# Performance work log

Measured on AMD Instinct MI355X. Metric: run time of the kernel, lower is better.

## Reference

```python
import jax, jax.numpy as jnp
import numpy as np
from jax import lax

B = 64            # batch size
IMG = 128         # image H=W
C_IN = 3          # channels (also conv kernel size in original code)
Q_DIM = 11
A_DIM = 10
CONV = [24, 24, 24, 24]
KS = 3
EPS = 1e-5
G_IN = (CONV[-1] + 2) * 2 + Q_DIM  # 63


def _lin_init(key, fin, fout):
    kw, kb = jax.random.split(key)
    w = jax.random.normal(kw, (fin, fout), jnp.float32) / np.sqrt(fin).astype(np.float32)
    b = jax.random.normal(kb, (fout,), jnp.float32) * 0.01
    return w, b


def _conv_init(key, cin, cout):
    kw, kb = jax.random.split(key)
    w = jax.random.normal(kw, (cout, cin, KS, KS), jnp.float32) / np.sqrt(cin * KS * KS).astype(np.float32)
    b = jax.random.normal(kb, (cout,), jnp.float32) * 0.01
    return w, b


def setup_inputs() -> dict:
    key = jax.random.key(0)
    ks = jax.random.split(key, 16)
    inp = {
        'img': jax.random.normal(ks[0], (B, C_IN, IMG, IMG), jnp.float32),
        'q': jax.random.normal(ks[1], (B, Q_DIM), jnp.float32),
    }
    cins = [C_IN] + CONV[:-1]
    for li in range(4):
        w, b = _conv_init(ks[2 + li], cins[li], CONV[li])
        inp[f'cw{li+1}'], inp[f'cb{li+1}'] = w, b
        inp[f'bg{li+1}'] = jnp.ones((CONV[li],), jnp.float32)
        inp[f'bb{li+1}'] = jnp.zeros((CONV[li],), jnp.float32)
    gins = [G_IN, 256, 256, 256]
    for li in range(4):
        w, b = _lin_init(ks[6 + li], gins[li], 256)
        inp[f'gw{li+1}'], inp[f'gb{li+1}'] = w, b
    fins, fouts = [256, 256, 256], [256, 256, A_DIM]
    for li in range(3):
        w, b = _lin_init(ks[10 + li], fins[li], fouts[li])
        inp[f'fw{li+1}'], inp[f'fb{li+1}'] = w, b
    return inp


def _conv_block(x, w, b, g, bb):
    # conv(stride=2, pad=1) -> relu -> batchnorm (train-mode batch stats)
    x = lax.conv_general_dilated(x, w, (2, 2), [(1, 1), (1, 1)],
                                 dimension_numbers=('NCHW', 'OIHW', 'NCHW'))
    x = jax.nn.relu(x + b[None, :, None, None])
    m = jnp.mean(x, axis=(0, 2, 3), keepdims=True)
    v = jnp.var(x, axis=(0, 2, 3), keepdims=True)
    return g[None, :, None, None] * (x - m) * jax.lax.rsqrt(v + EPS) + bb[None, :, None, None]


def _forward(img, q,
             cw1, cb1, bg1, bb1, cw2, cb2, bg2, bb2,
             cw3, cb3, bg3, bb3, cw4, cb4, bg4, bb4,
             gw1, gb1, gw2, gb2, gw3, gb3, gw4, gb4,
             fw1, fb1, fw2, fb2, fw3, fb3):
    x = _conv_block(img, cw1, cb1, bg1, bb1)
    x = _conv_block(x, cw2, cb2, bg2, bb2)
    x = _conv_block(x, cw3, cb3, bg3, bb3)
    x = _conv_block(x, cw4, cb4, bg4, bb4)        # [B, K, d, d]
    d = x.shape[2]
    N = d * d
    Kc = x.shape[1]
    # objects: o at flat index i corresponds to pixel (i//d, i%d) -> row-major reshape
    objs = x.reshape(B, Kc, N).transpose(0, 2, 1)           # [B, N, K]
    idx = jnp.arange(N)
    coords = jnp.stack([(idx // d).astype(jnp.float32) / d,
                        (idx % d).astype(jnp.float32) / d], axis=1)  # [N, 2]
    o = jnp.concatenate([objs, jnp.broadcast_to(coords[None], (B, N, 2))], axis=-1)  # [B, N, K+2]
    F = Kc + 2
    oi = jnp.broadcast_to(o[:, :, None, :], (B, N, N, F))
    oj = jnp.broadcast_to(o[:, None, :, :], (B, N, N, F))
    qb = jnp.broadcast_to(q[:, None, None, :], (B, N, N, Q_DIM))
    pair = jnp.concatenate([oi, oj, qb], axis=-1)           # [B, N, N, 2F+Q]
    h = jax.nn.relu(jnp.einsum('bijf,fh->bijh', pair, gw1) + gb1)
    h = jax.nn.relu(h @ gw2 + gb2)
    h = jax.nn.relu(h @ gw3 + gb3)
    h = jax.nn.relu(h @ gw4 + gb4)
    g = jnp.mean(h, axis=(1, 2))                            # mean over all N*N pairs -> [B, 256]
    # f_phi (dropout as identity / eval mode)
    g = jax.nn.relu(g @ fw1 + fb1)
    g = jax.nn.relu(g @ fw2 + fb2)
    logits = g @ fw3 + fb3
    return logits


def reference(img, q,
              cw1, cb1, bg1, bb1, cw2, cb2, bg2, bb2,
              cw3, cb3, bg3, bb3, cw4, cb4, bg4, bb4,
              gw1, gb1, gw2, gb2, gw3, gb3, gw4, gb4,
              fw1, fb1, fw2, fb2, fw3, fb3):
    return _forward(img, q,
                    cw1, cb1, bg1, bb1, cw2, cb2, bg2, bb2,
                    cw3, cb3, bg3, bb3, cw4, cb4, bg4, bb4,
                    gw1, gb1, gw2, gb2, gw3, gb3, gw4, gb4,
                    fw1, fb1, fw2, fb2, fw3, fb3)
```

## Files before the change

### kernel.cpp

```cpp
#include <hip/hip_runtime.h>
#include <hip/hip_bf16.h>

#define EPS_BN 1e-5f

typedef __bf16 bf16_t;
typedef __bf16 bf16x4 __attribute__((ext_vector_type(4)));
typedef __bf16 bf16x8 __attribute__((ext_vector_type(8)));
typedef float floatx16 __attribute__((ext_vector_type(16)));

__global__ __launch_bounds__(256) void prep_kernel(
    const float* __restrict__ q, const float* __restrict__ gw1,
    const float* __restrict__ gb1, const float* __restrict__ g2,
    const float* __restrict__ g3, const float* __restrict__ g4,
    float* __restrict__ wq, bf16_t* __restrict__ wpack)
{
    int blk = blockIdx.x, t = threadIdx.x;
    {
        float acc = gb1[t];
        #pragma unroll
        for (int d = 0; d < 11; d++)
            acc = fmaf(q[blk * 11 + d], gw1[(52 + d) * 256 + t], acc);
        wq[blk * 256 + t] = acc;
    }
    for (int idx = blk * 3072 + t; idx < blk * 3072 + 3072; idx += 256) {
        int layer = idx >> 16;
        int rem = idx & 65535;
        int col = rem & 255;
        int k = rem >> 8;
        const float* gw = (layer == 0) ? g2 : ((layer == 1) ? g3 : g4);
        float v = gw[k * 256 + col];
        int cg = col >> 5, l31 = col & 31;
        int kt = k >> 4, l2 = (k >> 3) & 1, e = k & 7;
        int lane = l2 * 32 + l31;
        wpack[(((layer * 8 + cg) * 16 + kt) * 64 + lane) * 8 + e] = (bf16_t)v;
    }
}

__global__ __launch_bounds__(256) void fin_kernel(
    const float* __restrict__ part, int P, float inv_n,
    const float* __restrict__ gamma, const float* __restrict__ beta,
    float* __restrict__ scsh)
{
    int c = blockIdx.x;
    int t = threadIdx.x;
    float s1 = 0.f, s2 = 0.f;
    for (int p = t; p < P; p += 256) {
        s1 += part[p * 48 + 2 * c];
        s2 += part[p * 48 + 2 * c + 1];
    }
    #pragma unroll
    for (int off = 32; off > 0; off >>= 1) {
        s1 += __shfl_xor(s1, off);
        s2 += __shfl_xor(s2, off);
    }
    __shared__ float r1[4], r2[4];
    int lane = t & 63, w = t >> 6;
    if (lane == 0) { r1[w] = s1; r2[w] = s2; }
    __syncthreads();
    if (t == 0) {
        float a1 = r1[0] + r1[1] + r1[2] + r1[3];
        float a2 = r2[0] + r2[1] + r2[2] + r2[3];
        float m = a1 * inv_n;
        float var = a2 * inv_n - m * m;
        float sc = gamma[c] * rsqrtf(var + EPS_BN);
        scsh[c] = sc;
        scsh[24 + c] = fmaf(-m, sc, beta[c]);
    }
}

template<int CIN, int HOUT, int OY_PER, int CO_PER, bool FOLD>
__global__ __launch_bounds__(256) void conv_kernel(
    const float* __restrict__ in, const float* __restrict__ scsh_in,
    const float* __restrict__ w, const float* __restrict__ bias,
    float* __restrict__ out, float* __restrict__ part_out)
{
    const int HIN = 2 * HOUT, ROWS = 2 * OY_PER + 3, RW = 2 * HOUT + 2;
    const int TILES = HOUT / OY_PER;
    const int WPC = (HOUT * OY_PER) / 64;
    int b = blockIdx.x / TILES, tile = blockIdx.x % TILES;
    int oy0 = tile * OY_PER;
    __shared__ float tin[CIN][ROWS][RW];
    __shared__ float scf[24], shf[24];
    __shared__ float red[4][CO_PER * 2];
    int t = threadIdx.x;
    if (FOLD) {
        if (t < 24) { scf[t] = scsh_in[t]; shf[t] = scsh_in[24 + t]; }
        __syncthreads();
    }
    const int total = CIN * ROWS * RW;
    int iyb = 2 * oy0 - 1;
    #pragma unroll 2
    for (int idx = t; idx < total; idx += 256) {
        int rx = idx % RW;
        int rem = idx / RW;
        int ry = rem % ROWS;
        int ci = rem / ROWS;
        int iy = iyb + ry, ix = rx - 1;
        float v = 0.f;
        if ((unsigned)iy < (unsigned)HIN && (unsigned)ix < (unsigned)HIN) {
            float raw = in[(b * CIN + ci) * HIN * HIN + iy * HIN + ix];
            v = FOLD ? fmaf(raw, scf[ci], shf[ci]) : raw;
        }
        tin[ci][ry][rx] = v;
    }
    __syncthreads();
    int ox = t % HOUT;
    int oyl = (t / HOUT) % OY_PER;
    int cog = t / (HOUT * OY_PER);
    const float* wp = w + cog * CO_PER * CIN * 9;
    float acc[CO_PER];
    #pragma unroll
    for (int r = 0; r < CO_PER; r++) acc[r] = bias[cog * CO_PER + r];
    for (int ci = 0; ci < CIN; ci++)
        #pragma unroll
        for (int ky = 0; ky < 3; ky++)
            #pragma unroll
            for (int kx = 0; kx < 3; kx++) {
                float v = tin[ci][2 * oyl + ky][2 * ox + kx];
                #pragma unroll
                for (int r = 0; r < CO_PER; r++)
                    acc[r] = fmaf(v, wp[(r * CIN + ci) * 9 + ky * 3 + kx], acc[r]);
            }
    int oy = oy0 + oyl;
    float s1[CO_PER], s2[CO_PER];
    #pragma unroll
    for (int r = 0; r < CO_PER; r++) {
        float v = fmaxf(acc[r], 0.f);
        out[((b * 24 + cog * CO_PER + r) * HOUT + oy) * HOUT + ox] = v;
        s1[r] = v;
        s2[r] = v * v;
    }
    int lane = t & 63, w_id = t >> 6;
    #pragma unroll
    for (int r = 0; r < CO_PER; r++) {
        float a = s1[r], c2 = s2[r];
        #pragma unroll
        for (int off = 32; off > 0; off >>= 1) {
            a += __shfl_xor(a, off);
            c2 += __shfl_xor(c2, off);
        }
        if (lane == 0) { red[w_id][r * 2] = a; red[w_id][r * 2 + 1] = c2; }
    }
    __syncthreads();
    if (t < 48) {
        int ch = t >> 1, st = t & 1;
        int cg = ch / CO_PER, r = ch % CO_PER;
        float v = 0.f;
        #pragma unroll
        for (int k = 0; k < WPC; k++) v += red[cg * WPC + k][r * 2 + st];
        part_out[blockIdx.x * 48 + t] = v;
    }
}

__global__ __launch_bounds__(256) void uv_kernel(
    const float* __restrict__ x4, const float* __restrict__ scsh4,
    const float* __restrict__ gw1, float* __restrict__ U, float* __restrict__ V)
{
    int b = blockIdx.x >> 2, n0 = (blockIdx.x & 3) * 16;
    __shared__ float o[16][26];
    int t = threadIdx.x;
    for (int idx = t; idx < 16 * 26; idx += 256) {
        int n = idx / 26, f = idx % 26;
        int ng = n0 + n;
        float val;
        if (f < 24)
            val = fmaf(x4[(b * 24 + f) * 64 + ng], scsh4[f], scsh4[24 + f]);
        else if (f == 24) val = (float)(ng >> 3) * 0.125f;
        else              val = (float)(ng & 7) * 0.125f;
        o[n][f] = val;
    }
    __syncthreads();
    float g1u[26], g1v[26];
    #pragma unroll
    for (int f = 0; f < 26; f++) {
        g1u[f] = gw1[f * 256 + t];
        g1v[f] = gw1[(26 + f) * 256 + t];
    }
    for (int n = 0; n < 16; n++) {
        float u = 0.f, v = 0.f;
        #pragma unroll
        for (int f = 0; f < 26; f++) {
            float of = o[n][f];
            u = fmaf(of, g1u[f], u);
            v = fmaf(of, g1v[f], v);
        }
        int ng = n0 + n;
        U[(b * 64 + ng) * 256 + t] = u;
        V[(b * 64 + ng) * 256 + t] = v;
    }
}

__global__ __launch_bounds__(256, 2) void pair_kernel(
    const float* __restrict__ U, const float* __restrict__ V,
    const float* __restrict__ wq, const bf16_t* __restrict__ wpack,
    const float* __restrict__ gb2, const float* __restrict__ gb3,
    const float* __restrict__ gb4, float* __restrict__ partial)
{
    __shared__ __align__(16) bf16_t hA[128][264];
    int blk = blockIdx.x;
    int b = blk >> 5;
    int i0 = (blk & 31) * 2;
    int t = threadIdx.x;

    {
        int c4 = (t & 63) * 4;
        int jh = t >> 6;
        float4 wq4 = *(const float4*)(wq + b * 256 + c4);
        float4 u0 = *(const float4*)(U + (b * 64 + i0) * 256 + c4);
        float4 u1 = *(const float4*)(U + (b * 64 + i0 + 1) * 256 + c4);
        u0.x += wq4.x; u0.y += wq4.y; u0.z += wq4.z; u0.w += wq4.w;
        u1.x += wq4.x; u1.y += wq4.y; u1.z += wq4.z; u1.w += wq4.w;
        const float* Vb = V + (b * 64) * 256 + c4;
        for (int j = jh * 16; j < jh * 16 + 16; j++) {
            float4 v = *(const float4*)(Vb + j * 256);
            bf16x4 h0, h1;
            h0[0] = (bf16_t)fmaxf(u0.x + v.x, 0.f);
            h0[1] = (bf16_t)fmaxf(u0.y + v.y, 0.f);
            h0[2] = (bf16_t)fmaxf(u0.z + v.z, 0.f);
            h0[3] = (bf16_t)fmaxf(u0.w + v.w, 0.f);
            h1[0] = (bf16_t)fmaxf(u1.x + v.x, 0.f);
            h1[1] = (bf16_t)fmaxf(u1.y + v.y, 0.f);
            h1[2] = (bf16_t)fmaxf(u1.z + v.z, 0.f);
            h1[3] = (bf16_t)fmaxf(u1.w + v.w, 0.f);
            *(bf16x4*)&hA[j][c4] = h0;
            *(bf16x4*)&hA[64 + j][c4] = h1;
        }
    }
    __syncthreads();

    int lane = t & 63, wn = t >> 6;
    int l31 = lane & 31, l2 = lane >> 5;

    #pragma unroll 1
    for (int layer = 0; layer < 2; layer++) {
        const float* bias = (layer == 0) ? gb2 : gb3;
        const bf16_t* W0 = wpack + ((size_t)((layer * 8 + wn * 2) * 1024) + lane) * 8;
        const bf16_t* W1 = W0 + 8192;

        floatx16 acc[4][2];
        #pragma unroll
        for (int nt = 0; nt < 2; nt++) {
            int fb = (wn * 2 + nt) * 32 + 4 * l2;
            #pragma unroll
            for (int g = 0; g < 4; g++) {
                float4 bv = *(const float4*)(bias + fb + 8 * g);
                acc[0][nt][4 * g + 0] = bv.x;
                acc[0][nt][4 * g + 1] = bv.y;
                acc[0][nt][4 * g + 2] = bv.z;
                acc[0][nt][4 * g + 3] = bv.w;
            }
            #pragma unroll
            for (int mt = 1; mt < 4; mt++) acc[mt][nt] = acc[0][nt];
        }

        bf16x8 Wb0[4], Wb1[4];
        #pragma unroll
        for (int p = 0; p < 4; p++) {
            Wb0[p] = *(const bf16x8*)(W0 + p * 512);
            Wb1[p] = *(const bf16x8*)(W1 + p * 512);
        }
        bf16x8 hb[2][4];
        #pragma unroll
        for (int mt = 0; mt < 4; mt++)
            hb[0][mt] = *(const bf16x8*)&hA[mt * 32 + l31][l2 * 8];

        #pragma unroll
        for (int ks = 0; ks < 16; ks++) {
            if (ks < 15) {
                #pragma unroll
                for (int mt = 0; mt < 4; mt++)
                    hb[(ks + 1) & 1][mt] =
                        *(const bf16x8*)&hA[mt * 32 + l31][(ks + 1) * 16 + l2 * 8];
            }
            #pragma unroll
            for (int mt = 0; mt < 4; mt++) {
                acc[mt][0] = __builtin_amdgcn_mfma_f32_32x32x16_bf16(Wb0[ks & 3], hb[ks & 1][mt], acc[mt][0], 0, 0, 0);
                acc[mt][1] = __builtin_amdgcn_mfma_f32_32x32x16_bf16(Wb1[ks & 3], hb[ks & 1][mt], acc[mt][1], 0, 0, 0);
            }
            if (ks + 4 < 16) {
                Wb0[ks & 3] = *(const bf16x8*)(W0 + (ks + 4) * 512);
                Wb1[ks & 3] = *(const bf16x8*)(W1 + (ks + 4) * 512);
            }
        }

        __syncthreads();
        #pragma unroll
        for (int mt = 0; mt < 4; mt++) {
            int row = mt * 32 + l31;
            #pragma unroll
            for (int nt = 0; nt < 2; nt++) {
                int fb = (wn * 2 + nt) * 32 + 4 * l2;
                #pragma unroll
                for (int g = 0; g < 4; g++) {
                    bf16x4 w4;
                    w4[0] = (bf16_t)fmaxf(acc[mt][nt][4 * g + 0], 0.f);
                    w4[1] = (bf16_t)fmaxf(acc[mt][nt][4 * g + 1], 0.f);
                    w4[2] = (bf16_t)fmaxf(acc[mt][nt][4 * g + 2], 0.f);
                    w4[3] = (bf16_t)fmaxf(acc[mt][nt][4 * g + 3], 0.f);
                    *(bf16x4*)&hA[row][fb + 8 * g] = w4;
                }
            }
        }
        __syncthreads();
    }

    {
        floatx16 acc[4][2];
        #pragma unroll
        for (int nt = 0; nt < 2; nt++) {
            float bc = gb4[wn * 64 + nt * 32 + l31];
            #pragma unroll
            for (int mt = 0; mt < 4; mt++)
                #pragma unroll
                for (int reg = 0; reg < 16; reg++)
                    acc[mt][nt][reg] = bc;
        }

        const bf16_t* W0 = wpack + ((size_t)((16 + wn * 2) * 1024) + lane) * 8;
        const bf16_t* W1 = W0 + 8192;

        bf16x8 Wb0[4], Wb1[4];
        #pragma unroll
        for (int p = 0; p < 4; p++) {
            Wb0[p] = *(const bf16x8*)(W0 + p * 512);
            Wb1[p] = *(const bf16x8*)(W1 + p * 512);
        }
        bf16x8 hb[2][4];
        #pragma unroll
        for (int mt = 0; mt < 4; mt++)
            hb[0][mt] = *(const bf16x8*)&hA[mt * 32 + l31][l2 * 8];

        #pragma unroll
        for (int ks = 0; ks < 16; ks++) {
            if (ks < 15) {
                #pragma unroll
                for (int mt = 0; mt < 4; mt++)
                    hb[(ks + 1) & 1][mt] =
                        *(const bf16x8*)&hA[mt * 32 + l31][(ks + 1) * 16 + l2 * 8];
            }
            #pragma unroll
            for (int mt = 0; mt < 4; mt++) {
                acc[mt][0] = __builtin_amdgcn_mfma_f32_32x32x16_bf16(hb[ks & 1][mt], Wb0[ks & 3], acc[mt][0], 0, 0, 0);
                acc[mt][1] = __builtin_amdgcn_mfma_f32_32x32x16_bf16(hb[ks & 1][mt], Wb1[ks & 3], acc[mt][1], 0, 0, 0);
            }
            if (ks + 4 < 16) {
                Wb0[ks & 3] = *(const bf16x8*)(W0 + (ks + 4) * 512);
                Wb1[ks & 3] = *(const bf16x8*)(W1 + (ks + 4) * 512);
            }
        }

        #pragma unroll
        for (int nt = 0; nt < 2; nt++) {
            float s = 0.f;
            #pragma unroll
            for (int mt = 0; mt < 4; mt++)
                #pragma unroll
                for (int reg = 0; reg < 16; reg++)
                    s += fmaxf(acc[mt][nt][reg], 0.0f);
            s += __shfl_xor(s, 32);
            if (l2 == 0)
                partial[blk * 256 + wn * 64 + nt * 32 + l31] = s;
        }
    }
}

__global__ __launch_bounds__(256) void fphi_kernel(
    const float* __restrict__ partial,
    const float* __restrict__ fw1, const float* __restrict__ fb1,
    const float* __restrict__ fw2, const float* __restrict__ fb2,
    const float* __restrict__ fw3, const float* __restrict__ fb3,
    float* __restrict__ out)
{
    int b = blockIdx.x, t = threadIdx.x;
    __shared__ float g[256], h1[256], h2[256];
    float s = 0.f;
    for (int k = 0; k < 32; k++) s += partial[(b * 32 + k) * 256 + t];
    g[t] = s * (1.0f / 4096.0f);
    __syncthreads();
    float a1 = fb1[t];
    for (int k = 0; k < 256; k++) a1 = fmaf(g[k], fw1[k * 256 + t], a1);
    h1[t] = fmaxf(a1, 0.0f);
    __syncthreads();
    float a2 = fb2[t];
    for (int k = 0; k < 256; k++) a2 = fmaf(h1[k], fw2[k * 256 + t], a2);
    h2[t] = fmaxf(a2, 0.0f);
    __syncthreads();
    if (t < 10) {
        float a3 = fb3[t];
        for (int k = 0; k < 256; k++) a3 = fmaf(h2[k], fw3[k * 10 + t], a3);
        out[b * 10 + t] = a3;
    }
}

extern "C" void kernel_launch(void* const* d_in, const int* in_sizes, int n_in,
                              void* d_out, int out_size, void* d_ws, size_t ws_size,
                              hipStream_t stream)
{
    (void)in_sizes; (void)n_in; (void)out_size; (void)ws_size;
    const float* img = (const float*)d_in[0];
    const float* q   = (const float*)d_in[1];
    const float* cw[4] = {(const float*)d_in[2],  (const float*)d_in[6],
                          (const float*)d_in[10], (const float*)d_in[14]};
    const float* cb[4] = {(const float*)d_in[3],  (const float*)d_in[7],
                          (const float*)d_in[11], (const float*)d_in[15]};
    const float* bg[4] = {(const float*)d_in[4],  (const float*)d_in[8],
                          (const float*)d_in[12], (const float*)d_in[16]};
    const float* bbv[4] = {(const float*)d_in[5],  (const float*)d_in[9],
                           (const float*)d_in[13], (const float*)d_in[17]};
    const float* gw1 = (const float*)d_in[18]; const float* gb1 = (const float*)d_in[19];
    const float* gw2 = (const float*)d_in[20]; const float* gb2 = (const float*)d_in[21];
    const float* gw3 = (const float*)d_in[22]; const float* gb3 = (const float*)d_in[23];
    const float* gw4 = (const float*)d_in[24]; const float* gb4 = (const float*)d_in[25];
    const float* fw1 = (const float*)d_in[26]; const float* fb1 = (const float*)d_in[27];
    const float* fw2 = (const float*)d_in[28]; const float* fb2 = (const float*)d_in[29];
    const float* fw3 = (const float*)d_in[30]; const float* fb3 = (const float*)d_in[31];

    float* ws  = (float*)d_ws;
    float* x1  = ws;
    float* x2  = x1 + 6291456;
    float* x3  = x2 + 1572864;
    float* x4  = x3 + 393216;
    float* U   = x4 + 98304;
    float* V   = U + 1048576;
    float* wqv = V + 1048576;
    float* part = wqv + 16384;
    float* p1  = part + 524288;
    float* p2  = p1 + 98304;
    float* p3  = p2 + 49152;
    float* p4  = p3 + 12288;
    float* scsh1 = p4 + 3072;
    float* scsh2 = scsh1 + 48;
    float* scsh3 = scsh2 + 48;
    float* scsh4 = scsh3 + 48;
    bf16_t* wpack = (bf16_t*)(scsh4 + 48);

    prep_kernel<<<64, 256, 0, stream>>>(q, gw1, gb1, gw2, gw3, gw4, wqv, wpack);
    conv_kernel<3, 64, 2, 12, false><<<2048, 256, 0, stream>>>(
        img, nullptr, cw[0], cb[0], x1, p1);
    fin_kernel<<<24, 256, 0, stream>>>(p1, 2048, 1.f / 262144.f, bg[0], bbv[0], scsh1);
    conv_kernel<24, 32, 2, 6, true><<<1024, 256, 0, stream>>>(
        x1, scsh1, cw[1], cb[1], x2, p2);
    fin_kernel<<<24, 256, 0, stream>>>(p2, 1024, 1.f / 65536.f, bg[1], bbv[1], scsh2);
    conv_kernel<24, 16, 4, 6, true><<<256, 256, 0, stream>>>(
        x2, scsh2, cw[2], cb[2], x3, p3);
    fin_kernel<<<24, 256, 0, stream>>>(p3, 256, 1.f / 16384.f, bg[2], bbv[2], scsh3);
    conv_kernel<24, 8, 8, 6, true><<<64, 256, 0, stream>>>(
        x3, scsh3, cw[3], cb[3], x4, p4);
    fin_kernel<<<24, 256, 0, stream>>>(p4, 64, 1.f / 4096.f, bg[3], bbv[3], scsh4);
    uv_kernel<<<256, 256, 0, stream>>>(x4, scsh4, gw1, U, V);
    pair_kernel<<<2048, 256, 0, stream>>>(U, V, wqv, wpack, gb2, gb3, gb4, part);
    fphi_kernel<<<64, 256, 0, stream>>>(part, fw1, fb1, fw2, fb2, fw3, fb3,
                                        (float*)d_out);
}
```

Measured before the change: 409.9 us.

## Fuse BN stat finalization into conv kernels via last-block atomic counter

Removes the four separate fin_kernel launches by having the last conv block, detected with an atomic counter and threadfence, reduce the partial sums and write the BN scale/shift. The prep work is folded into the first conv launch as extra blocks. The aim is to cut kernel launch and serialization overhead between the small stages. In exchange it adds an atomic, a memset and a serial tail reduction done by a single block.

```diff
diff --git a/kernel.cpp b/kernel.cpp
--- a/kernel.cpp
+++ b/kernel.cpp
@@ -8,81 +8,51 @@
 typedef __bf16 bf16x8 __attribute__((ext_vector_type(8)));
 typedef float floatx16 __attribute__((ext_vector_type(16)));
 
-__global__ __launch_bounds__(256) void prep_kernel(
-    const float* __restrict__ q, const float* __restrict__ gw1,
-    const float* __restrict__ gb1, const float* __restrict__ g2,
-    const float* __restrict__ g3, const float* __restrict__ g4,
-    float* __restrict__ wq, bf16_t* __restrict__ wpack)
-{
-    int blk = blockIdx.x, t = threadIdx.x;
-    {
-        float acc = gb1[t];
-        #pragma unroll
-        for (int d = 0; d < 11; d++)
-            acc = fmaf(q[blk * 11 + d], gw1[(52 + d) * 256 + t], acc);
-        wq[blk * 256 + t] = acc;
-    }
-    for (int idx = blk * 3072 + t; idx < blk * 3072 + 3072; idx += 256) {
-        int layer = idx >> 16;
-        int rem = idx & 65535;
-        int col = rem & 255;
-        int k = rem >> 8;
-        const float* gw = (layer == 0) ? g2 : ((layer == 1) ? g3 : g4);
-        float v = gw[k * 256 + col];
-        int cg = col >> 5, l31 = col & 31;
-        int kt = k >> 4, l2 = (k >> 3) & 1, e = k & 7;
-        int lane = l2 * 32 + l31;
-        wpack[(((layer * 8 + cg) * 16 + kt) * 64 + lane) * 8 + e] = (bf16_t)v;
-    }
-}
-
-__global__ __launch_bounds__(256) void fin_kernel(
-    const float* __restrict__ part, int P, float inv_n,
-    const float* __restrict__ gamma, const float* __restrict__ beta,
-    float* __restrict__ scsh)
-{
-    int c = blockIdx.x;
-    int t = threadIdx.x;
-    float s1 = 0.f, s2 = 0.f;
-    for (int p = t; p < P; p += 256) {
-        s1 += part[p * 48 + 2 * c];
-        s2 += part[p * 48 + 2 * c + 1];
-    }
-    #pragma unroll
-    for (int off = 32; off > 0; off >>= 1) {
-        s1 += __shfl_xor(s1, off);
-        s2 += __shfl_xor(s2, off);
-    }
-    __shared__ float r1[4], r2[4];
-    int lane = t & 63, w = t >> 6;
-    if (lane == 0) { r1[w] = s1; r2[w] = s2; }
-    __syncthreads();
-    if (t == 0) {
-        float a1 = r1[0] + r1[1] + r1[2] + r1[3];
-        float a2 = r2[0] + r2[1] + r2[2] + r2[3];
-        float m = a1 * inv_n;
-        float var = a2 * inv_n - m * m;
-        float sc = gamma[c] * rsqrtf(var + EPS_BN);
-        scsh[c] = sc;
-        scsh[24 + c] = fmaf(-m, sc, beta[c]);
-    }
-}
-
-template<int CIN, int HOUT, int OY_PER, int CO_PER, bool FOLD>
+template<int CIN, int HOUT, int OY_PER, int CO_PER, bool FOLD, bool PREP>
 __global__ __launch_bounds__(256) void conv_kernel(
     const float* __restrict__ in, const float* __restrict__ scsh_in,
     const float* __restrict__ w, const float* __restrict__ bias,
-    float* __restrict__ out, float* __restrict__ part_out)
+    float* __restrict__ out, float* __restrict__ part_out,
+    const float* __restrict__ gamma, const float* __restrict__ beta,
+    float* __restrict__ scsh_out, unsigned* __restrict__ counter,
+    const float* __restrict__ qv, const float* __restrict__ gw1v,
+    const float* __restrict__ gb1v, const float* __restrict__ g2v,
+    const float* __restrict__ g3v, const float* __restrict__ g4v,
+    float* __restrict__ wqo, bf16_t* __restrict__ wpck)
 {
     const int HIN = 2 * HOUT, ROWS = 2 * OY_PER + 3, RW = 2 * HOUT + 2;
     const int TILES = HOUT / OY_PER;
+    const int CONVBLKS = 64 * TILES;
     const int WPC = (HOUT * OY_PER) / 64;
+    int t = threadIdx.x;
+
+    if (PREP && blockIdx.x >= CONVBLKS) {
+        int blk = blockIdx.x - CONVBLKS;
+        float acc = gb1v[t];
+        #pragma unroll
+        for (int d = 0; d < 11; d++)
+            acc = fmaf(qv[blk * 11 + d], gw1v[(52 + d) * 256 + t], acc);
+        wqo[blk * 256 + t] = acc;
+        for (int idx = blk * 3072 + t; idx < blk * 3072 + 3072; idx += 256) {
+            int layer = idx >> 16;
+            int rem = idx & 65535;
+            int col = rem & 255;
+            int k = rem >> 8;
+            const float* gw = (layer == 0) ? g2v : ((layer == 1) ? g3v : g4v);
+            float v = gw[k * 256 + col];
+            int cg = col >> 5, l31x = col & 31;
+            int kt = k >> 4, l2x = (k >> 3) & 1, e = k & 7;
+            int lane2 = l2x * 32 + l31x;
+            wpck[(((layer * 8 + cg) * 16 + kt) * 64 + lane2) * 8 + e] = (bf16_t)v;
+        }
+        return;
+    }
+
     int b = blockIdx.x / TILES, tile = blockIdx.x % TILES;
     int oy0 = tile * OY_PER;
     __shared__ float tin[CIN][ROWS][RW];
     __shared__ float scf[24], shf[24];
     __shared__ float red[4][CO_PER * 2];
-    int t = threadIdx.x;
     if (FOLD) {
         if (t < 24) { scf[t] = scsh_in[t]; shf[t] = scsh_in[24 + t]; }
         __syncthreads();
@@ -150,6 +120,34 @@
         for (int k = 0; k < WPC; k++) v += red[cg * WPC + k][r * 2 + st];
         part_out[blockIdx.x * 48 + t] = v;
     }
+
+    __threadfence();
+    __syncthreads();
+    __shared__ unsigned lastflag;
+    if (t == 0)
+        lastflag = (atomicAdd(counter, 1u) == (unsigned)(CONVBLKS - 1)) ? 1u : 0u;
+    __syncthreads();
+    if (!lastflag) return;
+    __threadfence();
+    const float inv_n = 1.f / (float)(64 * HOUT * HOUT);
+    int s = t % 48, chk = t / 48;
+    float a = 0.f;
+    if (t < 240)
+        for (int p = chk; p < CONVBLKS; p += 5) a += part_out[p * 48 + s];
+    __shared__ float redf[5][48];
+    if (t < 240) redf[chk][s] = a;
+    __syncthreads();
+    if (t < 24) {
+        float sa = 0.f, sb = 0.f;
+        #pragma unroll
+        for (int k = 0; k < 5; k++) { sa += redf[k][2 * t]; sb += redf[k][2 * t + 1]; }
+        float m = sa * inv_n;
+        float var = sb * inv_n - m * m;
+        float sc = gamma[t] * rsqrtf(var + EPS_BN);
+        scsh_out[t] = sc;
+        scsh_out[24 + t] = fmaf(-m, sc, beta[t]);
+    }
+    if (t == 0) *counter = 0;
 }
 
 __global__ __launch_bounds__(256) void uv_kernel(
@@ -433,20 +431,26 @@
     float* scsh3 = scsh2 + 48;
     float* scsh4 = scsh3 + 48;
     bf16_t* wpack = (bf16_t*)(scsh4 + 48);
-
-    prep_kernel<<<64, 256, 0, stream>>>(q, gw1, gb1, gw2, gw3, gw4, wqv, wpack);
-    conv_kernel<3, 64, 2, 12, false><<<2048, 256, 0, stream>>>(
-        img, nullptr, cw[0], cb[0], x1, p1);
-    fin_kernel<<<24, 256, 0, stream>>>(p1, 2048, 1.f / 262144.f, bg[0], bbv[0], scsh1);
-    conv_kernel<24, 32, 2, 6, true><<<1024, 256, 0, stream>>>(
-        x1, scsh1, cw[1], cb[1], x2, p2);
-    fin_kernel<<<24, 256, 0, stream>>>(p2, 1024, 1.f / 65536.f, bg[1], bbv[1], scsh2);
-    conv_kernel<24, 16, 4, 6, true><<<256, 256, 0, stream>>>(
-        x2, scsh2, cw[2], cb[2], x3, p3);
-    fin_kernel<<<24, 256, 0, stream>>>(p3, 256, 1.f / 16384.f, bg[2], bbv[2], scsh3);
-    conv_kernel<24, 8, 8, 6, true><<<64, 256, 0, stream>>>(
-        x3, scsh3, cw[3], cb[3], x4, p4);
-    fin_kernel<<<24, 256, 0, stream>>>(p4, 64, 1.f / 4096.f, bg[3], bbv[3], scsh4);
+    unsigned* ctrs = (unsigned*)(wpack + 196608);
+
+    hipMemsetAsync(ctrs, 0, 4 * sizeof(unsigned), stream);
+
+    conv_kernel<3, 64, 2, 12, false, true><<<2048 + 64, 256, 0, stream>>>(
+        img, nullptr, cw[0], cb[0], x1, p1,
+        bg[0], bbv[0], scsh1, ctrs + 0,
+        q, gw1, gb1, gw2, gw3, gw4, wqv, wpack);
+    conv_kernel<24, 32, 2, 6, true, false><<<1024, 256, 0, stream>>>(
+        x1, scsh1, cw[1], cb[1], x2, p2,
+        bg[1], bbv[1], scsh2, ctrs + 1,
+        nullptr, nullptr, nullptr, nullptr, nullptr, nullptr, nullptr, nullptr);
+    conv_kernel<24, 16, 4, 6, true, false><<<256, 256, 0, stream>>>(
+        x2, scsh2, cw[2], cb[2], x3, p3,
+        bg[2], bbv[2], scsh3, ctrs + 2,
+        nullptr, nullptr, nullptr, nullptr, nullptr, nullptr, nullptr, nullptr);
+    conv_kernel<24, 8, 8, 6, true, false><<<64, 256, 0, stream>>>(
+        x3, scsh3, cw[3], cb[3], x4, p4,
+        bg[3], bbv[3], scsh4, ctrs + 3,
+        nullptr, nullptr, nullptr, nullptr, nullptr, nullptr, nullptr, nullptr);
     uv_kernel<<<256, 256, 0, stream>>>(x4, scsh4, gw1, U, V);
     pair_kernel<<<2048, 256, 0, stream>>>(U, V, wqv, wpack, gb2, gb3, gb4, part);
     fphi_kernel<<<64, 256, 0, stream>>>(part, fw1, fb1, fw2, fb2, fw3, fb3,
```

Result: slower. 780.4 us (+90.4%).
